# Performance work log

Measured on AMD Instinct MI355X. Metric: run time of the kernel, lower is better.

The kernel has to match this reference:

```python
import jax, jax.numpy as jnp
import numpy as np

# Fixed problem dims (see shape_source)
B, N_PER, K, D_IN, D_H, N_LAYERS = 4, 8192, 20, 128, 128, 3
N = B * N_PER


def setup_inputs() -> dict:
    key = jax.random.key(0)
    ks = jax.random.split(key, 6)
    x = jax.random.normal(ks[0], (N, D_IN), jnp.float32)
    pos = jax.random.normal(ks[1], (N, 3), jnp.float32)
    batch = jnp.repeat(jnp.arange(B, dtype=jnp.int32), N_PER)  # sorted, equal-size graphs
    sc = lambda k, sh: jax.random.normal(k, sh, jnp.float32) * 0.05
    # TriConv layer i: MLP(Linear(in+3 -> hidden), ReLU, Linear(hidden -> hidden)),
    # messages summed at target nodes. in == hidden == 128 so weights stack cleanly.
    W1s = sc(ks[2], (N_LAYERS, D_IN + 3, D_H))
    b1s = jnp.zeros((N_LAYERS, D_H), jnp.float32)
    W2s = sc(ks[3], (N_LAYERS, D_H, D_H))
    b2s = jnp.zeros((N_LAYERS, D_H), jnp.float32)
    Wf = sc(ks[4], (D_H, 1))
    bf = jnp.zeros((1,), jnp.float32)
    return {"x": x, "pos": pos, "batch": batch, "W1s": W1s, "b1s": b1s,
            "W2s": W2s, "b2s": b2s, "Wf": Wf, "bf": bf}


def knn_graph(pos):
    """Faithful, vectorized version of custom_knn_graph for equal-size graphs.
    Returns fixed-size (src, dst, mask); mask zeroes exact-duplicate edges,
    mirroring torch.unique(edge_index, dim=1) for sum aggregation."""
    posb = pos.reshape(B, N_PER, 3)

    def per_batch(p):
        d2 = jnp.sum((p[:, None, :] - p[None, :, :]) ** 2, axis=-1)  # [n,n]; same order as cdist
        d2 = jnp.where(jnp.eye(N_PER, dtype=bool), jnp.inf, d2)      # fill_diagonal_(inf)
        _, idx = jax.lax.top_k(-d2, K)                               # k smallest
        return idx

    idx = jax.vmap(per_batch)(posb)                                   # [B, n, k]
    off = (jnp.arange(B) * N_PER)[:, None, None]
    dst = (idx + off).reshape(-1)
    src = jnp.broadcast_to(jnp.arange(N_PER)[None, :, None] + off, idx.shape).reshape(-1)
    # symmetrize: cat([e, e.flip(0)])
    s = jnp.concatenate([src, dst])
    t = jnp.concatenate([dst, src])
    # dedup (torch.unique over edge columns) via sort + first-occurrence mask
    keys = s * N + t                                                  # fits in int32 (N=2^15)
    order = jnp.argsort(keys)
    ksort = keys[order]
    first = jnp.concatenate([jnp.array([True]), ksort[1:] != ksort[:-1]])
    mask = jnp.zeros_like(first).at[order].set(first)
    return s, t, mask


def reference(x, pos, batch, W1s, b1s, W2s, b2s, Wf, bf):
    if pos.ndim == 3:
        pos = pos.mean(axis=1)
    src, dst, mask = knn_graph(pos)
    w = mask.astype(x.dtype)[:, None]
    for i in range(N_LAYERS):
        rel = pos[dst] - pos[src]                                     # pos_i - pos_j, [E,3]
        m = jnp.concatenate([x[src], rel], axis=-1)                   # [E, d+3]
        m = jax.nn.relu(m @ W1s[i] + b1s[i]) @ W2s[i] + b2s[i]        # edge MLP
        x = jax.ops.segment_sum(m * w, dst, num_segments=N)           # sum-aggregate at targets
        x = jax.nn.relu(x)
    logits = (x @ Wf + bf)[:, 0]                                      # [N]
    # scatter_softmax over batch == per-graph softmax (equal-size graphs)
    probs = jax.nn.softmax(logits.reshape(B, N_PER), axis=1)
    return probs.reshape(-1)
```

## Files before the change

kernel.cpp:

```cpp
#include <hip/hip_runtime.h>
#include <stdint.h>

#define N_NODES 32768
#define NPER    8192
#define NB      4
#define KK      20
#define DH      128

typedef unsigned long long u64;
typedef unsigned short ushort;

__device__ __forceinline__ ushort f2bf(float f) {
  unsigned x = __float_as_uint(f);
  return (ushort)((x + 0x7fff + ((x >> 16) & 1)) >> 16);
}
__device__ __forceinline__ float bflo(unsigned u) { return __uint_as_float(u << 16); }
__device__ __forceinline__ float bfhi(unsigned u) { return __uint_as_float(u & 0xffff0000u); }

__device__ __forceinline__ u64 shflx64(u64 x, int m) {
  unsigned lo = __shfl_xor((unsigned)(x & 0xffffffffu), m, 64);
  unsigned hi = __shfl_xor((unsigned)(x >> 32), m, 64);
  return (((u64)hi) << 32) | lo;
}
__device__ __forceinline__ u64 shfl64(u64 x, int src) {
  unsigned lo = __shfl((unsigned)(x & 0xffffffffu), src, 64);
  unsigned hi = __shfl((unsigned)(x >> 32), src, 64);
  return (((u64)hi) << 32) | lo;
}
__device__ __forceinline__ int mbcnt64(u64 mask) {
  return __builtin_amdgcn_mbcnt_hi((unsigned)(mask >> 32),
         __builtin_amdgcn_mbcnt_lo((unsigned)mask, 0u));
}
__device__ __forceinline__ u64 bsort64(u64 key, int lane) {
#pragma unroll
  for (int k = 2; k <= 64; k <<= 1) {
#pragma unroll
    for (int j = k >> 1; j >= 1; j >>= 1) {
      u64 other = shflx64(key, j);
      bool up = ((lane & k) == 0);
      bool keepmin = (((lane & j) == 0) == up);
      bool take = keepmin ? (other < key) : (other > key);
      key = take ? other : key;
    }
  }
  return key;
}
__device__ __forceinline__ unsigned bsortu32(unsigned key, int lane) {
#pragma unroll
  for (int k = 2; k <= 64; k <<= 1) {
#pragma unroll
    for (int j = k >> 1; j >= 1; j >>= 1) {
      unsigned other = (unsigned)__shfl_xor((int)key, j, 64);
      bool up = ((lane & k) == 0);
      bool keepmin = (((lane & j) == 0) == up);
      bool take = keepmin ? (other < key) : (other > key);
      key = take ? other : key;
    }
  }
  return key;
}
__device__ __forceinline__ u64 bclean64(u64 key, int lane) {
#pragma unroll
  for (int j = 32; j >= 1; j >>= 1) {
    u64 other = shflx64(key, j);
    bool keepmin = ((lane & j) == 0);
    bool take = keepmin ? (other < key) : (other > key);
    key = take ? other : key;
  }
  return key;
}

__device__ __forceinline__ void compact64(u64* bufr, int& cnt, u64& lo,
                                          unsigned& thr, int lane) {
  asm volatile("s_waitcnt lgkmcnt(0)" ::: "memory");
  u64 k = (lane < cnt) ? bufr[lane] : ~0ull;
  k = bsort64(k, lane);
  u64 kr = shfl64(k, 63 - lane);
  u64 m = (kr < lo) ? kr : lo;
  lo = bclean64(m, lane);
  thr = (unsigned)(shfl64(lo, KK) >> 32);
  cnt = 0;
  asm volatile("s_waitcnt lgkmcnt(0)" ::: "memory");
}

__global__ __launch_bounds__(256) void knn_kernel(const float* __restrict__ pos,
                                                  int* __restrict__ knn)
{
  __shared__ u64 buf[8][64];

  const int lane = threadIdx.x & 63;
  const int w    = threadIdx.x >> 6;
  const int rowA = blockIdx.x * 8 + w * 2;
  const int rowB = rowA + 1;
  const int base = (rowA >> 13) << 13;

  const float ax = pos[rowA*3+0], ay = pos[rowA*3+1], az = pos[rowA*3+2];
  const float bx = pos[rowB*3+0], by = pos[rowB*3+1], bz = pos[rowB*3+2];

  unsigned thra, thrb;
  int cnta = 0, cntb = 0;
  u64 loa = ~0ull, lob = ~0ull;
  u64* bufa = buf[w*2+0];
  u64* bufb = buf[w*2+1];

  const float4* __restrict__ p4 = (const float4*)(pos + (size_t)base*3);

  {
    float4 q0 = p4[lane*3+0];
    float4 q1 = p4[lane*3+1];
    float4 q2 = p4[lane*3+2];
    const float X[4] = {q0.x, q0.w, q1.z, q2.y};
    const float Y[4] = {q0.y, q1.x, q1.w, q2.z};
    const float Z[4] = {q0.z, q1.y, q2.x, q2.w};
    float mA = 3.4e38f, mB = 3.4e38f;
#pragma unroll
    for (int r = 0; r < 4; r++) {
      float dx = ax - X[r], dy = ay - Y[r], dz = az - Z[r];
      mA = fminf(mA, fmaf(dx, dx, fmaf(dy, dy, dz*dz)));
      float ex = bx - X[r], ey = by - Y[r], ez = bz - Z[r];
      mB = fminf(mB, fmaf(ex, ex, fmaf(ey, ey, ez*ez)));
    }
    unsigned sA = bsortu32(__float_as_uint(mA), lane);
    unsigned sB = bsortu32(__float_as_uint(mB), lane);
    thra = (unsigned)__shfl((int)sA, KK, 64);
    thrb = (unsigned)__shfl((int)sB, KK, 64);
  }

  for (int it = 0; it < 32; it++) {
    const int c0 = it*256 + lane*4;
    const int f4 = it*192 + lane*3;
    float4 q0 = p4[f4+0];
    float4 q1 = p4[f4+1];
    float4 q2 = p4[f4+2];
    const float X[4] = {q0.x, q0.w, q1.z, q2.y};
    const float Y[4] = {q0.y, q1.x, q1.w, q2.z};
    const float Z[4] = {q0.z, q1.y, q2.x, q2.w};

    float dA[4], dB[4];
#pragma unroll
    for (int r = 0; r < 4; r++) {
      float dx = ax - X[r], dy = ay - Y[r], dz = az - Z[r];
      dA[r] = fmaf(dx, dx, fmaf(dy, dy, dz*dz));
      float ex = bx - X[r], ey = by - Y[r], ez = bz - Z[r];
      dB[r] = fmaf(ex, ex, fmaf(ey, ey, ez*ez));
    }
    float mnA = fminf(fminf(dA[0], dA[1]), fminf(dA[2], dA[3]));
    float mnB = fminf(fminf(dB[0], dB[1]), fminf(dB[2], dB[3]));

    if (__any(__float_as_uint(mnA) <= thra)) {
#pragma unroll
      for (int r = 0; r < 4; r++) {
        unsigned bits = __float_as_uint(dA[r]);
        bool pred = (bits <= thra);
        u64 mask = __ballot(pred);
        int pc = __popcll(mask);
        if (cnta + pc > 64) compact64(bufa, cnta, loa, thra, lane);
        if (pred) bufa[cnta + mbcnt64(mask)] =
            (((u64)bits) << 32) | (unsigned)(base + c0 + r);
        cnta = __builtin_amdgcn_readfirstlane(cnta + pc);
      }
    }
    if (__any(__float_as_uint(mnB) <= thrb)) {
#pragma unroll
      for (int r = 0; r < 4; r++) {
        unsigned bits = __float_as_uint(dB[r]);
        bool pred = (bits <= thrb);
        u64 mask = __ballot(pred);
        int pc = __popcll(mask);
        if (cntb + pc > 64) compact64(bufb, cntb, lob, thrb, lane);
        if (pred) bufb[cntb + mbcnt64(mask)] =
            (((u64)bits) << 32) | (unsigned)(base + c0 + r);
        cntb = __builtin_amdgcn_readfirstlane(cntb + pc);
      }
    }
  }
  compact64(bufa, cnta, loa, thra, lane);
  compact64(bufb, cntb, lob, thrb, lane);

  {
    u64 ball = __ballot(((int)(loa & 0xffffffffu) == rowA) && (lane <= KK));
    int p0 = __ffsll((long long)ball) - 1;
    if (p0 < 0) p0 = KK + 1;
    int src = lane + ((lane >= p0) ? 1 : 0);
    u64 outk = shfl64(loa, src);
    if (lane < KK) knn[rowA*KK + lane] = (int)(outk & 0xffffffffu);
  }
  {
    u64 ball = __ballot(((int)(lob & 0xffffffffu) == rowB) && (lane <= KK));
    int p0 = __ffsll((long long)ball) - 1;
    if (p0 < 0) p0 = KK + 1;
    int src = lane + ((lane >= p0) ? 1 : 0);
    u64 outk = shfl64(lob, src);
    if (lane < KK) knn[rowB*KK + lane] = (int)(outk & 0xffffffffu);
  }
}

__global__ void pos4_kernel(const float* __restrict__ pos, float4* __restrict__ pos4)
{
  int i = blockIdx.x * 256 + threadIdx.x;
  if (i >= N_NODES) return;
  pos4[i] = make_float4(pos[i*3+0], pos[i*3+1], pos[i*3+2], 0.f);
}

__global__ void count_kernel(const int* __restrict__ knn, int* __restrict__ flags,
                             int* __restrict__ cnt)
{
  int e = blockIdx.x * 256 + threadIdx.x;
  if (e >= N_NODES*KK) return;
  int i = e / KK;
  int d = knn[e];
  int mut = 0;
#pragma unroll
  for (int t = 0; t < KK; t++) mut |= (knn[d*KK + t] == i);
  flags[e] = mut;
  if (!mut) atomicAdd(&cnt[d], 1);
}

__global__ __launch_bounds__(1024) void scan_kernel(const int* __restrict__ cnt,
                                                    int* __restrict__ off)
{
  __shared__ int ssum[1024];
  int tid = threadIdx.x;
  int i0 = tid * 32;
  int loc[32];
  int s = 0;
#pragma unroll
  for (int j = 0; j < 32; j++) { loc[j] = s; s += cnt[i0 + j]; }
  ssum[tid] = s;
  __syncthreads();
  for (int d = 1; d < 1024; d <<= 1) {
    int t = (tid >= d) ? ssum[tid - d] : 0;
    __syncthreads();
    ssum[tid] += t;
    __syncthreads();
  }
  int bse = ssum[tid] - s;
#pragma unroll
  for (int j = 0; j < 32; j++) off[i0 + j] = bse + loc[j];
  if (tid == 1023) off[N_NODES] = bse + s;
}

__global__ void fill_kernel(const int* __restrict__ knn, const int* __restrict__ flags,
                            const int* __restrict__ off, int* __restrict__ cursor,
                            int* __restrict__ extra)
{
  int e = blockIdx.x * 256 + threadIdx.x;
  if (e >= N_NODES*KK) return;
  if (flags[e]) return;
  int i = e / KK;
  int d = knn[e];
  int p = atomicAdd(&cursor[d], 1);
  extra[off[d] + p] = i;
}

template<int RELU, int DEG, int OBF16>
__global__ __launch_bounds__(256) void gemm128(const float* __restrict__ X,
    const float* __restrict__ W, const float* __restrict__ bias,
    const int* __restrict__ offs, void* __restrict__ Yv)
{
  __shared__ float ws[128*128];
  const int tid = threadIdx.x;
  const int p   = blockIdx.x;
  const int g   = (p & 7) >> 1;
  const int j   = ((p >> 3) << 1) | (p & 1);
  const int r0  = g*NPER + j*64;

  {
    const float4* W4 = (const float4*)W;
    float4* ws4 = (float4*)ws;
#pragma unroll
    for (int li = 0; li < 16; li++) ws4[tid + li*256] = W4[tid + li*256];
  }
  __syncthreads();

  const int tr = tid >> 4, tc = tid & 15;
  const int rr0 = tr*4, cc0 = tc*8;
  float acc[4][8];
#pragma unroll
  for (int a = 0; a < 4; a++)
#pragma unroll
    for (int c = 0; c < 8; c++) acc[a][c] = 0.f;

  for (int kc = 0; kc < 32; kc++) {
    float4 xr[4];
#pragma unroll
    for (int rr = 0; rr < 4; rr++)
      xr[rr] = *(const float4*)&X[(size_t)(r0 + rr0 + rr)*128 + kc*4];
#pragma unroll
    for (int kk = 0; kk < 4; kk++) {
      float4 wA = *(const float4*)&ws[(kc*4 + kk)*128 + cc0];
      float4 wB = *(const float4*)&ws[(kc*4 + kk)*128 + cc0 + 4];
      float wv[8] = {wA.x, wA.y, wA.z, wA.w, wB.x, wB.y, wB.z, wB.w};
      float xa[4] = {kk==0?xr[0].x:kk==1?xr[0].y:kk==2?xr[0].z:xr[0].w,
                     kk==0?xr[1].x:kk==1?xr[1].y:kk==2?xr[1].z:xr[1].w,
                     kk==0?xr[2].x:kk==1?xr[2].y:kk==2?xr[2].z:xr[2].w,
                     kk==0?xr[3].x:kk==1?xr[3].y:kk==2?xr[3].z:xr[3].w};
#pragma unroll
      for (int rr = 0; rr < 4; rr++)
#pragma unroll
        for (int cc = 0; cc < 8; cc++) acc[rr][cc] += xa[rr] * wv[cc];
    }
  }
#pragma unroll
  for (int rr = 0; rr < 4; rr++) {
    int r = r0 + rr0 + rr;
    float dg = 1.f;
    if (DEG) dg = (float)(KK + offs[r+1] - offs[r]);
    float o[8];
#pragma unroll
    for (int cc = 0; cc < 8; cc++) {
      float vv = acc[rr][cc] + bias[cc0+cc] * dg;
      if (RELU) vv = fmaxf(vv, 0.f);
      o[cc] = vv;
    }
    if (OBF16) {
      ushort* Y = (ushort*)Yv;
      unsigned pk[4];
#pragma unroll
      for (int q = 0; q < 4; q++)
        pk[q] = (unsigned)f2bf(o[2*q]) | ((unsigned)f2bf(o[2*q+1]) << 16);
      *(uint4*)&Y[(size_t)r*128 + cc0] = make_uint4(pk[0], pk[1], pk[2], pk[3]);
    } else {
      float* Y = (float*)Yv;
      *(float4*)&Y[(size_t)r*128 + cc0]     = make_float4(o[0], o[1], o[2], o[3]);
      *(float4*)&Y[(size_t)r*128 + cc0 + 4] = make_float4(o[4], o[5], o[6], o[7]);
    }
  }
}

__global__ __launch_bounds__(256) void agg_kernel(const ushort* __restrict__ H,
    const float4* __restrict__ pos4, const int* __restrict__ knn,
    const int* __restrict__ off, const int* __restrict__ extra,
    const float* __restrict__ Wr, float* __restrict__ agg)
{
  const int lane = threadIdx.x & 63;
  const int w    = threadIdx.x >> 6;
  const int grp  = lane >> 4;
  const int hl   = lane & 15;
  const int dblk = blockIdx.x;
  const int g    = (dblk >> 1) & 3;
  const int nb   = ((dblk >> 3) << 1) | (dblk & 1);
  const int d    = g*NPER + nb*16 + w*4 + grp;
  const int c0   = hl * 8;

  const int4* kn4 = (const int4*)&knn[d*KK];
  int4 i0 = kn4[0], i1 = kn4[1], i2 = kn4[2], i3 = kn4[3], i4 = kn4[4];
  const int e0 = off[d], e1 = off[d+1];
  const int idx[KK] = {i0.x,i0.y,i0.z,i0.w, i1.x,i1.y,i1.z,i1.w,
                       i2.x,i2.y,i2.z,i2.w, i3.x,i3.y,i3.z,i3.w,
                       i4.x,i4.y,i4.z,i4.w};

  float w0[8], w1[8], w2[8];
#pragma unroll
  for (int jj = 0; jj < 8; jj++) {
    w0[jj] = Wr[0*DH + c0 + jj];
    w1[jj] = Wr[1*DH + c0 + jj];
    w2[jj] = Wr[2*DH + c0 + jj];
  }
  const float4 pd = pos4[d];
  const float px = pd.x, py = pd.y, pz = pd.z;

  float a[8];
#pragma unroll
  for (int jj = 0; jj < 8; jj++) a[jj] = 0.f;

#pragma unroll
  for (int t = 0; t < KK; t++) {
    int s = idx[t];
    float4 ps = pos4[s];
    float rx = px - ps.x, ry = py - ps.y, rz = pz - ps.z;
    uint4 hv = *(const uint4*)&H[(size_t)s*DH + c0];
    float h[8] = {bflo(hv.x), bfhi(hv.x), bflo(hv.y), bfhi(hv.y),
                  bflo(hv.z), bfhi(hv.z), bflo(hv.w), bfhi(hv.w)};
#pragma unroll
    for (int jj = 0; jj < 8; jj++) {
      float m = h[jj] + rx*w0[jj] + ry*w1[jj] + rz*w2[jj];
      a[jj] += fmaxf(m, 0.f);
    }
  }
  for (int t = e0; t < e1; t++) {
    int s = extra[t];
    float4 ps = pos4[s];
    float rx = px - ps.x, ry = py - ps.y, rz = pz - ps.z;
    uint4 hv = *(const uint4*)&H[(size_t)s*DH + c0];
    float h[8] = {bflo(hv.x), bfhi(hv.x), bflo(hv.y), bfhi(hv.y),
                  bflo(hv.z), bfhi(hv.z), bflo(hv.w), bfhi(hv.w)};
#pragma unroll
    for (int jj = 0; jj < 8; jj++) {
      float m = h[jj] + rx*w0[jj] + ry*w1[jj] + rz*w2[jj];
      a[jj] += fmaxf(m, 0.f);
    }
  }
  *(float4*)&agg[(size_t)d*DH + c0]     = make_float4(a[0], a[1], a[2], a[3]);
  *(float4*)&agg[(size_t)d*DH + c0 + 4] = make_float4(a[4], a[5], a[6], a[7]);
}

__global__ __launch_bounds__(256) void logits_kernel(const float* __restrict__ X,
    const float* __restrict__ Wf, const float* __restrict__ bf,
    float* __restrict__ logits)
{
  const int n = blockIdx.x * 256 + threadIdx.x;
  const float4* xr = (const float4*)&X[(size_t)n*128];
  float acc = 0.f;
#pragma unroll 8
  for (int q = 0; q < 32; q++) {
    float4 xv = xr[q];
    float4 wv = *(const float4*)&Wf[q*4];
    acc += xv.x*wv.x + xv.y*wv.y + xv.z*wv.z + xv.w*wv.w;
  }
  logits[n] = acc + bf[0];
}

__global__ __launch_bounds__(1024) void softmax_kernel(const float* __restrict__ logits,
    float* __restrict__ out)
{
  __shared__ float red[16];
  __shared__ float bcast;
  const int g = blockIdx.x, tid = threadIdx.x;
  const int lane = tid & 63, wid = tid >> 6;
  float lg[8];
#pragma unroll
  for (int k = 0; k < 8; k++) lg[k] = logits[g*NPER + k*1024 + tid];
  float m = lg[0];
#pragma unroll
  for (int k = 1; k < 8; k++) m = fmaxf(m, lg[k]);
  for (int o = 1; o < 64; o <<= 1) m = fmaxf(m, __shfl_xor(m, o, 64));
  if (lane == 0) red[wid] = m;
  __syncthreads();
  if (tid == 0) {
    float mm = red[0];
    for (int i = 1; i < 16; i++) mm = fmaxf(mm, red[i]);
    bcast = mm;
  }
  __syncthreads();
  const float M = bcast;
  float e[8];
  float s = 0.f;
#pragma unroll
  for (int k = 0; k < 8; k++) { e[k] = expf(lg[k] - M); s += e[k]; }
  for (int o = 1; o < 64; o <<= 1) s += __shfl_xor(s, o, 64);
  __syncthreads();
  if (lane == 0) red[wid] = s;
  __syncthreads();
  if (tid == 0) {
    float ss = 0.f;
    for (int i = 0; i < 16; i++) ss += red[i];
    bcast = ss;
  }
  __syncthreads();
  const float S = bcast;
#pragma unroll
  for (int k = 0; k < 8; k++) {
    int n = g*NPER + k*1024 + tid;
    out[n] = e[k] / S;
  }
}

extern "C" void kernel_launch(void* const* d_in, const int* in_sizes, int n_in,
                              void* d_out, int out_size, void* d_ws, size_t ws_size,
                              hipStream_t stream)
{
  const float* x   = (const float*)d_in[0];
  const float* pos = (const float*)d_in[1];
  const float* W1s = (const float*)d_in[3];
  const float* b1s = (const float*)d_in[4];
  const float* W2s = (const float*)d_in[5];
  const float* b2s = (const float*)d_in[6];
  const float* Wf  = (const float*)d_in[7];
  const float* bf  = (const float*)d_in[8];
  float* out = (float*)d_out;

  char* wsb = (char*)d_ws;
  size_t o = 0;
  auto alloc = [&](size_t bytes) { void* p = wsb + o; o += (bytes + 255) & ~255ull; return p; };
  int*    knn    = (int*)   alloc((size_t)N_NODES*KK*4);
  int*    flags  = (int*)   alloc((size_t)N_NODES*KK*4);
  int*    cnt    = (int*)   alloc((size_t)(N_NODES+1)*4);
  int*    off    = (int*)   alloc((size_t)(N_NODES+1)*4);
  int*    cursor = (int*)   alloc((size_t)N_NODES*4);
  int*    extra  = (int*)   alloc((size_t)N_NODES*KK*4);
  ushort* H      = (ushort*)alloc((size_t)N_NODES*DH*2);
  float*  agg    = (float*) alloc((size_t)N_NODES*DH*4);
  float*  xbuf   = (float*) alloc((size_t)N_NODES*DH*4);
  float4* pos4   = (float4*)alloc((size_t)N_NODES*16);
  float*  logits = (float*) alloc((size_t)N_NODES*4);
  (void)ws_size; (void)in_sizes; (void)n_in; (void)out_size;

  hipMemsetAsync(cnt,    0, (size_t)(N_NODES+1)*4, stream);
  hipMemsetAsync(cursor, 0, (size_t)N_NODES*4,     stream);

  knn_kernel <<<N_NODES/8, 256, 0, stream>>>(pos, knn);
  pos4_kernel<<<N_NODES/256, 256, 0, stream>>>(pos, pos4);
  count_kernel<<<(N_NODES*KK + 255)/256, 256, 0, stream>>>(knn, flags, cnt);
  scan_kernel<<<1, 1024, 0, stream>>>(cnt, off);
  fill_kernel<<<(N_NODES*KK + 255)/256, 256, 0, stream>>>(knn, flags, off, cursor, extra);

  const float* xin = x;
  for (int l = 0; l < 3; l++) {
    const float* W1 = W1s + (size_t)l*131*128;
    const float* Wr = W1 + 128*128;
    const float* b1 = b1s + l*128;
    const float* W2 = W2s + (size_t)l*128*128;
    const float* b2 = b2s + l*128;
    gemm128<0,0,1><<<N_NODES/64, 256, 0, stream>>>(xin, W1, b1, nullptr, H);
    agg_kernel  <<<N_NODES/16, 256, 0, stream>>>(H, pos4, knn, off, extra, Wr, agg);
    gemm128<1,1,0><<<N_NODES/64, 256, 0, stream>>>(agg, W2, b2, off, xbuf);
    xin = xbuf;
  }
  logits_kernel <<<N_NODES/256, 256, 0, stream>>>(xbuf, Wf, bf, logits);
  softmax_kernel<<<NB, 1024, 0, stream>>>(logits, out);
}
```

Before: 415.4 us.

## Replace brute-force KNN with uniform grid spatial hashing and shell search

Points are binned into a per-graph 32^3 uniform grid via counting sort (cell ids, scan, reorder into sorted float4 positions). Each wavefront then scans cells in expanding shells around its query, maintaining the top-K buffer. It stops once the shell distance bound exceeds the current K-th distance. This removes the all-pairs distance work per graph, at the cost of extra setup kernels, atomics, and irregular per-query work that depends on the point distribution.

```diff
diff --git a/kernel.cpp b/kernel.cpp
--- a/kernel.cpp
+++ b/kernel.cpp
@@ -6,6 +6,11 @@
 #define NB      4
 #define KK      20
 #define DH      128
+#define GRID    32
+#define NCELLS  (GRID*GRID*GRID)
+#define GMIN    (-6.5f)
+#define GINV    (32.0f/13.0f)
+#define CEDGE   0.40625f
 
 typedef unsigned long long u64;
 typedef unsigned short ushort;
@@ -45,20 +50,6 @@
   }
   return key;
 }
-__device__ __forceinline__ unsigned bsortu32(unsigned key, int lane) {
-#pragma unroll
-  for (int k = 2; k <= 64; k <<= 1) {
-#pragma unroll
-    for (int j = k >> 1; j >= 1; j >>= 1) {
-      unsigned other = (unsigned)__shfl_xor((int)key, j, 64);
-      bool up = ((lane & k) == 0);
-      bool keepmin = (((lane & j) == 0) == up);
-      bool take = keepmin ? (other < key) : (other > key);
-      key = take ? other : key;
-    }
-  }
-  return key;
-}
 __device__ __forceinline__ u64 bclean64(u64 key, int lane) {
 #pragma unroll
   for (int j = 32; j >= 1; j >>= 1) {
@@ -69,7 +60,6 @@
   }
   return key;
 }
-
 __device__ __forceinline__ void compact64(u64* bufr, int& cnt, u64& lo,
                                           unsigned& thr, int lane) {
   asm volatile("s_waitcnt lgkmcnt(0)" ::: "memory");
@@ -83,116 +73,133 @@
   asm volatile("s_waitcnt lgkmcnt(0)" ::: "memory");
 }
 
-__global__ __launch_bounds__(256) void knn_kernel(const float* __restrict__ pos,
-                                                  int* __restrict__ knn)
-{
-  __shared__ u64 buf[8][64];
-
+
+__global__ void cellid_kernel(const float* __restrict__ pos,
+                              int* __restrict__ cellId, int* __restrict__ cellCnt)
+{
+  int i = blockIdx.x * 256 + threadIdx.x;
+  if (i >= N_NODES) return;
+  float x = pos[i*3+0], y = pos[i*3+1], z = pos[i*3+2];
+  int cx = min(max((int)((x - GMIN) * GINV), 0), GRID-1);
+  int cy = min(max((int)((y - GMIN) * GINV), 0), GRID-1);
+  int cz = min(max((int)((z - GMIN) * GINV), 0), GRID-1);
+  int c = ((i >> 13) << 15) + (cz*GRID + cy)*GRID + cx;
+  cellId[i] = c;
+  atomicAdd(&cellCnt[c], 1);
+}
+
+__global__ __launch_bounds__(1024) void cellscan_kernel(const int* __restrict__ cnt,
+                                                        int* __restrict__ off)
+{
+  __shared__ int ssum[1024];
+  const int gbase = blockIdx.x << 15;
+  const int tid = threadIdx.x;
+  const int i0 = tid * 32;
+  int loc[32];
+  int s = 0;
+#pragma unroll
+  for (int j = 0; j < 32; j++) { loc[j] = s; s += cnt[gbase + i0 + j]; }
+  ssum[tid] = s;
+  __syncthreads();
+  for (int d = 1; d < 1024; d <<= 1) {
+    int t = (tid >= d) ? ssum[tid - d] : 0;
+    __syncthreads();
+    ssum[tid] += t;
+    __syncthreads();
+  }
+  int bse = ssum[tid] - s + blockIdx.x * NPER;
+#pragma unroll
+  for (int j = 0; j < 32; j++) off[gbase + i0 + j] = bse + loc[j];
+  if (blockIdx.x == 3 && tid == 1023) off[4*NCELLS] = N_NODES;
+}
+
+__global__ void reorder_kernel(const float* __restrict__ pos,
+                               const int* __restrict__ cellId,
+                               const int* __restrict__ off, int* __restrict__ cursor,
+                               float4* __restrict__ sortedPos)
+{
+  int i = blockIdx.x * 256 + threadIdx.x;
+  if (i >= N_NODES) return;
+  int c = cellId[i];
+  int slot = atomicAdd(&cursor[c], 1);
+  sortedPos[off[c] + slot] =
+      make_float4(pos[i*3+0], pos[i*3+1], pos[i*3+2], __int_as_float(i));
+}
+
+__global__ __launch_bounds__(256) void knn_grid_kernel(
+    const float4* __restrict__ pos4, const float4* __restrict__ sortedPos,
+    const int* __restrict__ cellOff, int* __restrict__ knn)
+{
+  __shared__ u64 buf[4][64];
   const int lane = threadIdx.x & 63;
   const int w    = threadIdx.x >> 6;
-  const int rowA = blockIdx.x * 8 + w * 2;
-  const int rowB = rowA + 1;
-  const int base = (rowA >> 13) << 13;
-
-  const float ax = pos[rowA*3+0], ay = pos[rowA*3+1], az = pos[rowA*3+2];
-  const float bx = pos[rowB*3+0], by = pos[rowB*3+1], bz = pos[rowB*3+2];
-
-  unsigned thra, thrb;
-  int cnta = 0, cntb = 0;
-  u64 loa = ~0ull, lob = ~0ull;
-  u64* bufa = buf[w*2+0];
-  u64* bufb = buf[w*2+1];
-
-  const float4* __restrict__ p4 = (const float4*)(pos + (size_t)base*3);
-
-  {
-    float4 q0 = p4[lane*3+0];
-    float4 q1 = p4[lane*3+1];
-    float4 q2 = p4[lane*3+2];
-    const float X[4] = {q0.x, q0.w, q1.z, q2.y};
-    const float Y[4] = {q0.y, q1.x, q1.w, q2.z};
-    const float Z[4] = {q0.z, q1.y, q2.x, q2.w};
-    float mA = 3.4e38f, mB = 3.4e38f;
-#pragma unroll
-    for (int r = 0; r < 4; r++) {
-      float dx = ax - X[r], dy = ay - Y[r], dz = az - Z[r];
-      mA = fminf(mA, fmaf(dx, dx, fmaf(dy, dy, dz*dz)));
-      float ex = bx - X[r], ey = by - Y[r], ez = bz - Z[r];
-      mB = fminf(mB, fmaf(ex, ex, fmaf(ey, ey, ez*ez)));
-    }
-    unsigned sA = bsortu32(__float_as_uint(mA), lane);
-    unsigned sB = bsortu32(__float_as_uint(mB), lane);
-    thra = (unsigned)__shfl((int)sA, KK, 64);
-    thrb = (unsigned)__shfl((int)sB, KK, 64);
-  }
-
-  for (int it = 0; it < 32; it++) {
-    const int c0 = it*256 + lane*4;
-    const int f4 = it*192 + lane*3;
-    float4 q0 = p4[f4+0];
-    float4 q1 = p4[f4+1];
-    float4 q2 = p4[f4+2];
-    const float X[4] = {q0.x, q0.w, q1.z, q2.y};
-    const float Y[4] = {q0.y, q1.x, q1.w, q2.z};
-    const float Z[4] = {q0.z, q1.y, q2.x, q2.w};
-
-    float dA[4], dB[4];
-#pragma unroll
-    for (int r = 0; r < 4; r++) {
-      float dx = ax - X[r], dy = ay - Y[r], dz = az - Z[r];
-      dA[r] = fmaf(dx, dx, fmaf(dy, dy, dz*dz));
-      float ex = bx - X[r], ey = by - Y[r], ez = bz - Z[r];
-      dB[r] = fmaf(ex, ex, fmaf(ey, ey, ez*ez));
-    }
-    float mnA = fminf(fminf(dA[0], dA[1]), fminf(dA[2], dA[3]));
-    float mnB = fminf(fminf(dB[0], dB[1]), fminf(dB[2], dB[3]));
-
-    if (__any(__float_as_uint(mnA) <= thra)) {
-#pragma unroll
-      for (int r = 0; r < 4; r++) {
-        unsigned bits = __float_as_uint(dA[r]);
-        bool pred = (bits <= thra);
-        u64 mask = __ballot(pred);
-        int pc = __popcll(mask);
-        if (cnta + pc > 64) compact64(bufa, cnta, loa, thra, lane);
-        if (pred) bufa[cnta + mbcnt64(mask)] =
-            (((u64)bits) << 32) | (unsigned)(base + c0 + r);
-        cnta = __builtin_amdgcn_readfirstlane(cnta + pc);
+  const int node = blockIdx.x * 4 + w;
+  const int cellBase = (node >> 13) << 15;
+
+  const float4 qp = pos4[node];
+  const float px = qp.x, py = qp.y, pz = qp.z;
+  const int cx = min(max((int)((px - GMIN) * GINV), 0), GRID-1);
+  const int cy = min(max((int)((py - GMIN) * GINV), 0), GRID-1);
+  const int cz = min(max((int)((pz - GMIN) * GINV), 0), GRID-1);
+
+  unsigned thr = 0xffffffffu;
+  int cnt = 0;
+  u64 lo = ~0ull;
+  u64* bufr = buf[w];
+
+  for (int D = 0; D < GRID; D++) {
+    const int z0 = max(cz - D, 0), z1 = min(cz + D, GRID-1);
+    for (int z = z0; z <= z1; z++) {
+      const int adz = (z > cz) ? (z - cz) : (cz - z);
+      const int y0 = max(cy - D, 0), y1 = min(cy + D, GRID-1);
+      for (int y = y0; y <= y1; y++) {
+        const int ady = (y > cy) ? (y - cy) : (cy - y);
+        const int rowBase = cellBase + (z*GRID + y)*GRID;
+        int pstart, pend, pstart2 = 0, pend2 = 0;
+        if (adz == D || ady == D) {
+          int x0 = max(cx - D, 0), x1 = min(cx + D, GRID-1);
+          pstart = cellOff[rowBase + x0];
+          pend   = cellOff[rowBase + x1 + 1];
+        } else {
+          pstart = 0; pend = 0;
+          if (cx - D >= 0)      { int c = rowBase + cx - D; pstart  = cellOff[c]; pend  = cellOff[c+1]; }
+          if (cx + D <= GRID-1) { int c = rowBase + cx + D; pstart2 = cellOff[c]; pend2 = cellOff[c+1]; }
+        }
+#pragma unroll
+        for (int half = 0; half < 2; half++) {
+          int ps = half ? pstart2 : pstart;
+          int pe = half ? pend2   : pend;
+          for (int ib = ps; ib < pe; ib += 64) {
+            int i = ib + lane;
+            bool valid = (i < pe);
+            float4 sp = sortedPos[valid ? i : ps];
+            float dx = px - sp.x, dy = py - sp.y, dz = pz - sp.z;
+            float d2 = fmaf(dx, dx, fmaf(dy, dy, dz*dz));
+            unsigned bits = __float_as_uint(d2);
+            bool pred = valid && (bits <= thr);
+            u64 mask = __ballot(pred);
+            if (mask) {
+              int pc = __popcll(mask);
+              if (cnt + pc > 64) compact64(bufr, cnt, lo, thr, lane);
+              if (pred) bufr[cnt + mbcnt64(mask)] =
+                  (((u64)bits) << 32) | __float_as_uint(sp.w);
+              cnt = __builtin_amdgcn_readfirstlane(cnt + pc);
+            }
+          }
+        }
       }
     }
-    if (__any(__float_as_uint(mnB) <= thrb)) {
-#pragma unroll
-      for (int r = 0; r < 4; r++) {
-        unsigned bits = __float_as_uint(dB[r]);
-        bool pred = (bits <= thrb);
-        u64 mask = __ballot(pred);
-        int pc = __popcll(mask);
-        if (cntb + pc > 64) compact64(bufb, cntb, lob, thrb, lane);
-        if (pred) bufb[cntb + mbcnt64(mask)] =
-            (((u64)bits) << 32) | (unsigned)(base + c0 + r);
-        cntb = __builtin_amdgcn_readfirstlane(cntb + pc);
-      }
-    }
-  }
-  compact64(bufa, cnta, loa, thra, lane);
-  compact64(bufb, cntb, lob, thrb, lane);
-
-  {
-    u64 ball = __ballot(((int)(loa & 0xffffffffu) == rowA) && (lane <= KK));
-    int p0 = __ffsll((long long)ball) - 1;
-    if (p0 < 0) p0 = KK + 1;
-    int src = lane + ((lane >= p0) ? 1 : 0);
-    u64 outk = shfl64(loa, src);
-    if (lane < KK) knn[rowA*KK + lane] = (int)(outk & 0xffffffffu);
-  }
-  {
-    u64 ball = __ballot(((int)(lob & 0xffffffffu) == rowB) && (lane <= KK));
-    int p0 = __ffsll((long long)ball) - 1;
-    if (p0 < 0) p0 = KK + 1;
-    int src = lane + ((lane >= p0) ? 1 : 0);
-    u64 outk = shfl64(lob, src);
-    if (lane < KK) knn[rowB*KK + lane] = (int)(outk & 0xffffffffu);
-  }
+    compact64(bufr, cnt, lo, thr, lane);
+    float bound = (float)D * CEDGE;
+    if (thr <= __float_as_uint(bound * bound)) break;
+  }
+
+  u64 ball = __ballot(((int)(lo & 0xffffffffu) == node) && (lane <= KK));
+  int p0 = __ffsll((long long)ball) - 1;
+  if (p0 < 0) p0 = KK + 1;
+  int src = lane + ((lane >= p0) ? 1 : 0);
+  u64 outk = shfl64(lo, src);
+  if (lane < KK) knn[node*KK + lane] = (int)(outk & 0xffffffffu);
 }
 
 __global__ void pos4_kernel(const float* __restrict__ pos, float4* __restrict__ pos4)
@@ -484,13 +491,24 @@
   float*  xbuf   = (float*) alloc((size_t)N_NODES*DH*4);
   float4* pos4   = (float4*)alloc((size_t)N_NODES*16);
   float*  logits = (float*) alloc((size_t)N_NODES*4);
+  int*    cellId = (int*)   alloc((size_t)N_NODES*4);
+  int*    cellCnt= (int*)   alloc((size_t)4*NCELLS*4);
+  int*    cellOff= (int*)   alloc((size_t)(4*NCELLS+1)*4);
+  int*    cellCur= (int*)   alloc((size_t)4*NCELLS*4);
+  float4* spos   = (float4*)alloc((size_t)N_NODES*16);
   (void)ws_size; (void)in_sizes; (void)n_in; (void)out_size;
 
-  hipMemsetAsync(cnt,    0, (size_t)(N_NODES+1)*4, stream);
-  hipMemsetAsync(cursor, 0, (size_t)N_NODES*4,     stream);
-
-  knn_kernel <<<N_NODES/8, 256, 0, stream>>>(pos, knn);
-  pos4_kernel<<<N_NODES/256, 256, 0, stream>>>(pos, pos4);
+  hipMemsetAsync(cnt,     0, (size_t)(N_NODES+1)*4, stream);
+  hipMemsetAsync(cursor,  0, (size_t)N_NODES*4,     stream);
+  hipMemsetAsync(cellCnt, 0, (size_t)4*NCELLS*4,    stream);
+  hipMemsetAsync(cellCur, 0, (size_t)4*NCELLS*4,    stream);
+
+  pos4_kernel   <<<N_NODES/256, 256, 0, stream>>>(pos, pos4);
+  cellid_kernel <<<N_NODES/256, 256, 0, stream>>>(pos, cellId, cellCnt);
+  cellscan_kernel<<<4, 1024, 0, stream>>>(cellCnt, cellOff);
+  reorder_kernel<<<N_NODES/256, 256, 0, stream>>>(pos, cellId, cellOff, cellCur, spos);
+  knn_grid_kernel<<<N_NODES/4, 256, 0, stream>>>(pos4, spos, cellOff, knn);
+
   count_kernel<<<(N_NODES*KK + 255)/256, 256, 0, stream>>>(knn, flags, cnt);
   scan_kernel<<<1, 1024, 0, stream>>>(cnt, off);
   fill_kernel<<<(N_NODES*KK + 255)/256, 256, 0, stream>>>(knn, flags, off, cursor, extra);
```

After: 530.7 us. 27.8% more time.
